# Kernel optimization log

Hardware: AMD Instinct MI355X
Metric: run time of the kernel (lower is better)

The kernel has to match this reference:

```python
import jax, jax.numpy as jnp
import numpy as np

EMBED_DIM = 2048
N_HEADS = 16
D_HEAD = EMBED_DIM // N_HEADS


def setup_inputs() -> dict:
    key = jax.random.key(0)
    kx, kq, kk, kv = jax.random.split(key, 4)
    B, N, D = 4, 2048, EMBED_DIM
    x = jax.random.normal(kx, (B, N, D), dtype=jnp.float32)
    Wq = jax.random.normal(kq, (D, D), dtype=jnp.float32) * 0.02
    Wk = jax.random.normal(kk, (D, D), dtype=jnp.float32) * 0.02
    Wv = jax.random.normal(kv, (D, D), dtype=jnp.float32) * 0.02
    return {"x": x, "Wq": Wq, "Wk": Wk, "Wv": Wv}


def reference(x, Wq, Wk, Wv):
    # x: [B, N, D]; weights applied as x @ W (matching torch.matmul in source)
    B, N, D = x.shape
    H, d = N_HEADS, D_HEAD
    # [B, N, D] -> [B, H, N, d]
    Q = (x @ Wq).reshape(B, N, H, d).transpose(0, 2, 1, 3)
    K = (x @ Wk).reshape(B, N, H, d).transpose(0, 2, 1, 3)
    V = (x @ Wv).reshape(B, N, H, d).transpose(0, 2, 1, 3)
    scale = 1.0 / jnp.sqrt(jnp.asarray(d, dtype=x.dtype))
    # non-causal SDPA (torch default: no mask, scale = 1/sqrt(d_head))
    scores = jnp.einsum('bhqd,bhkd->bhqk', Q, K) * scale  # [B,H,N,N]
    attn = jax.nn.softmax(scores, axis=-1)
    out = jnp.einsum('bhqk,bhkd->bhqd', attn, V)  # [B,H,N,d]
    return out
```

## Files before the change

### kernel.cpp

```cpp
#include <hip/hip_runtime.h>
#include <hip/hip_bf16.h>

#define B 4
#define N 2048
#define D 2048
#define H 16
#define DH 128
#define NT 32

typedef unsigned short u16;
typedef __attribute__((ext_vector_type(8))) short short8;
typedef __attribute__((ext_vector_type(4))) float floatx4;

__device__ __forceinline__ u16 f2b(float f) {
    union { __hip_bfloat16 h; u16 u; } cv;
    cv.h = __float2bfloat16(f);
    return cv.u;
}

__device__ __forceinline__ floatx4 mfma16(short8 a, short8 b, floatx4 c) {
    return __builtin_amdgcn_mfma_f32_16x16x32_bf16(a, b, c, 0, 0, 0);
}

#if __has_builtin(__builtin_amdgcn_exp2f)
#define EXP2(x) __builtin_amdgcn_exp2f(x)
#else
#define EXP2(x) exp2f(x)
#endif

__device__ __forceinline__ void async16(const void* g, void* l) {
    __builtin_amdgcn_global_load_lds(
        (const __attribute__((address_space(1))) unsigned int*)g,
        (__attribute__((address_space(3))) unsigned int*)l, 16, 0, 0);
}

__global__ __launch_bounds__(256) void cvt_x(const float* __restrict__ x,
                                             u16* __restrict__ xb) {
    size_t i = ((size_t)blockIdx.x * 256 + threadIdx.x) * 8;
    float4 v0 = *(const float4*)&x[i];
    float4 v1 = *(const float4*)&x[i + 4];
    union { u16 u[8]; uint4 s; } pk;
    pk.u[0] = f2b(v0.x); pk.u[1] = f2b(v0.y); pk.u[2] = f2b(v0.z); pk.u[3] = f2b(v0.w);
    pk.u[4] = f2b(v1.x); pk.u[5] = f2b(v1.y); pk.u[6] = f2b(v1.z); pk.u[7] = f2b(v1.w);
    *(uint4*)&xb[i] = pk.s;
}

__global__ __launch_bounds__(256) void cvt_w_t(const float* __restrict__ Wq,
                                               const float* __restrict__ Wk,
                                               const float* __restrict__ Wv,
                                               u16* __restrict__ wt) {
    __shared__ float tile[64][65];
    const int z = blockIdx.z;
    const float* W = (z == 0) ? Wq : (z == 1) ? Wk : Wv;
    const float scl = (z == 0) ? 0.12751743342f : 1.0f;
    const int k0 = blockIdx.x * 64, n0 = blockIdx.y * 64;
    const int tr = threadIdx.x >> 4, tc = threadIdx.x & 15;
#pragma unroll
    for (int i = 0; i < 4; i++) {
        int kk = tr + 16 * i;
        float4 vv = *(const float4*)&W[(size_t)(k0 + kk) * D + n0 + tc * 4];
        tile[kk][tc * 4 + 0] = vv.x; tile[kk][tc * 4 + 1] = vv.y;
        tile[kk][tc * 4 + 2] = vv.z; tile[kk][tc * 4 + 3] = vv.w;
    }
    __syncthreads();
#pragma unroll
    for (int i = 0; i < 4; i++) {
        int nn = tr + 16 * i;
        union { u16 u[4]; ushort4 s; } pk;
#pragma unroll
        for (int j = 0; j < 4; j++) pk.u[j] = f2b(tile[tc * 4 + j][nn] * scl);
        *(ushort4*)&wt[(size_t)z * D * D + (size_t)(n0 + nn) * D + k0 + tc * 4] = pk.s;
    }
}

#define KT 32
#define SGB __builtin_amdgcn_sched_group_barrier
__global__ __launch_bounds__(512, 2) void qkv_gemm(const u16* __restrict__ xb,
                                                   const u16* __restrict__ wt,
                                                   u16* __restrict__ qo,
                                                   u16* __restrict__ ko,
                                                   u16* __restrict__ vo) {
    __shared__ u16 lds[81920];

    const int bid = blockIdx.x;
    const int c = bid & 7, i = bid >> 3;
    const int i6 = (i * 43) >> 8;
    const int tm = ((c >> 2) << 4) + i6;
    const int tn = (c & 3) * 6 + (i - 6 * i6);

    const int t = threadIdx.x, lane = t & 63, w = t >> 6;
    const int wr = w >> 2, wc = w & 3;
    const int q4 = lane >> 4, lr = lane & 15;

    const int m0 = tm * 256;
    const int n0 = tn * 256;

    unsigned aoff[2][2], boff[2][2];
#pragma unroll
    for (int ii = 0; ii < 2; ii++) {
        const int off = ii * 8192 + w * 1024 + lane * 16;
        const int row = off >> 7;
        const int s = (off >> 4) & 7;
        const int col = ((s ^ (row & 7))) * 8;
#pragma unroll
        for (int h = 0; h < 2; h++) {
            aoff[h][ii] = (unsigned)((m0 + h * 128 + row) * D + col);
            boff[h][ii] = (unsigned)((n0 + h * 128 + row) * D + col);
        }
    }

    const unsigned cb0 = (unsigned)(((0 * 4 + q4) ^ (lr & 7)) * 16);
    const unsigned cb1 = (unsigned)(((1 * 4 + q4) ^ (lr & 7)) * 16);
    const unsigned aC0 = (unsigned)(wr * 16384 + lr * 128) + cb0;
    const unsigned aC1 = (unsigned)(wr * 16384 + lr * 128) + cb1;
    const unsigned bC0 = (unsigned)((wc >> 1) * 16384 + (wc & 1) * 8192 + lr * 128) + cb0;
    const unsigned bC1 = (unsigned)((wc >> 1) * 16384 + (wc & 1) * 8192 + lr * 128) + cb1;

#define STAGE_A(bufoff, h, j) {                                                           \
    async16(xb + aoff[h][0] + (unsigned)(j) * 64,                                         \
            (char*)lds + (bufoff) + (h) * 16384 + w * 1024);                              \
    async16(xb + aoff[h][1] + (unsigned)(j) * 64,                                         \
            (char*)lds + (bufoff) + (h) * 16384 + 8192 + w * 1024); }
#define STAGE_B(bufoff, h, j) {                                                           \
    async16(wt + boff[h][0] + (unsigned)(j) * 64,                                         \
            (char*)lds + (bufoff) + (h) * 16384 + w * 1024);                              \
    async16(wt + boff[h][1] + (unsigned)(j) * 64,                                         \
            (char*)lds + (bufoff) + (h) * 16384 + 8192 + w * 1024); }
#define BAR() __builtin_amdgcn_s_barrier()
#define DSR(off) (*(const short8*)((const char*)lds + (off)))

    floatx4 acc[8][4];
#pragma unroll
    for (int x = 0; x < 8; x++)
#pragma unroll
        for (int j = 0; j < 4; j++) acc[x][j] = (floatx4){0.f, 0.f, 0.f, 0.f};

    STAGE_A(0u, 0, 0); STAGE_A(0u, 1, 0);
    STAGE_B(98304u, 0, 0); STAGE_B(98304u, 1, 0);
    STAGE_A(32768u, 0, 1); STAGE_A(32768u, 1, 1);
    asm volatile("s_waitcnt vmcnt(4)" ::: "memory");
    BAR();

    unsigned aOffR = 0u;
    unsigned aOffW = 65536u;

    for (int g = 0; g < KT; g++) {
        const unsigned bR = 98304u + (unsigned)((g & 1) << 15);
        const unsigned bW = 98304u + (unsigned)(((g + 1) & 1) << 15);

        if (g + 1 < KT) { STAGE_B(bW, 0, g + 1); STAGE_B(bW, 1, g + 1); }
        if (g + 2 < KT) { STAGE_A(aOffW, 0, g + 2); STAGE_A(aOffW, 1, g + 2); }
        __builtin_amdgcn_sched_barrier(0);

        const unsigned aB0 = aOffR + aC0, aB1 = aOffR + aC1;
        const unsigned bB0 = bR + bC0, bB1 = bR + bC1;

        short8 a0k0[4], a0k1[4], a1k0[4], a1k1[4];
        short8 b0k0[2], b0k1[2], b1k0[2], b1k1[2];

        b0k0[0] = DSR(bB0);        b0k0[1] = DSR(bB0 + 2048);
#pragma unroll
        for (int mf = 0; mf < 4; mf++) a0k0[mf] = DSR(aB0 + mf * 2048);
#pragma unroll
        for (int mf = 0; mf < 4; mf++) a1k0[mf] = DSR(aB0 + 8192 + mf * 2048);
#pragma unroll
        for (int nf = 0; nf < 2; nf++)
#pragma unroll
            for (int mf = 0; mf < 4; mf++)
                acc[mf][nf] = mfma16(a0k0[mf], b0k0[nf], acc[mf][nf]);
        b1k0[0] = DSR(bB0 + 4096); b1k0[1] = DSR(bB0 + 6144);
#pragma unroll
        for (int nf = 0; nf < 2; nf++)
#pragma unroll
            for (int mf = 0; mf < 4; mf++)
                acc[4 + mf][nf] = mfma16(a1k0[mf], b0k0[nf], acc[4 + mf][nf]);
        b0k1[0] = DSR(bB1);        b0k1[1] = DSR(bB1 + 2048);
#pragma unroll
        for (int mf = 0; mf < 4; mf++) a0k1[mf] = DSR(aB1 + mf * 2048);
#pragma unroll
        for (int nf = 0; nf < 2; nf++)
#pragma unroll
            for (int mf = 0; mf < 4; mf++)
                acc[4 + mf][2 + nf] = mfma16(a1k0[mf], b1k0[nf], acc[4 + mf][2 + nf]);
#pragma unroll
        for (int mf = 0; mf < 4; mf++) a1k1[mf] = DSR(aB1 + 8192 + mf * 2048);
#pragma unroll
        for (int nf = 0; nf < 2; nf++)
#pragma unroll
            for (int mf = 0; mf < 4; mf++)
                acc[mf][2 + nf] = mfma16(a0k0[mf], b1k0[nf], acc[mf][2 + nf]);
        b1k1[0] = DSR(bB1 + 4096); b1k1[1] = DSR(bB1 + 6144);
#pragma unroll
        for (int nf = 0; nf < 2; nf++)
#pragma unroll
            for (int mf = 0; mf < 4; mf++)
                acc[mf][nf] = mfma16(a0k1[mf], b0k1[nf], acc[mf][nf]);
#pragma unroll
        for (int nf = 0; nf < 2; nf++)
#pragma unroll
            for (int mf = 0; mf < 4; mf++)
                acc[4 + mf][nf] = mfma16(a1k1[mf], b0k1[nf], acc[4 + mf][nf]);
#pragma unroll
        for (int nf = 0; nf < 2; nf++)
#pragma unroll
            for (int mf = 0; mf < 4; mf++)
                acc[4 + mf][2 + nf] = mfma16(a1k1[mf], b1k1[nf], acc[4 + mf][2 + nf]);
#pragma unroll
        for (int nf = 0; nf < 2; nf++)
#pragma unroll
            for (int mf = 0; mf < 4; mf++)
                acc[mf][2 + nf] = mfma16(a0k1[mf], b1k1[nf], acc[mf][2 + nf]);

        SGB(0x100, 10, 0);
        SGB(0x008,  8, 0);
        SGB(0x100,  2, 0);
        SGB(0x008,  8, 0);
        SGB(0x100,  6, 0);
        SGB(0x008,  8, 0);
        SGB(0x100,  4, 0);
        SGB(0x008,  8, 0);
        SGB(0x100,  2, 0);
        SGB(0x008,  8, 0);
        SGB(0x008,  8, 0);
        SGB(0x008,  8, 0);
        SGB(0x008,  8, 0);

        if (g == KT - 2) { asm volatile("s_waitcnt vmcnt(0)" ::: "memory"); }
        else if (g < KT - 2) { asm volatile("s_waitcnt vmcnt(4)" ::: "memory"); }
        if (g + 1 < KT) BAR();

        aOffR = (aOffR == 65536u) ? 0u : aOffR + 32768u;
        aOffW = (aOffW == 65536u) ? 0u : aOffW + 32768u;
    }

    const int z = tn >> 3;
    u16* dst = (z == 0) ? qo : (z == 1) ? ko : vo;
    const int c2b = (tn & 7) * 256 + wc * 64;
    const int grb = tm * 256 + wr * 128;
#pragma unroll
    for (int mf = 0; mf < 8; mf++)
#pragma unroll
        for (int nf = 0; nf < 4; nf++)
#pragma unroll
            for (int r = 0; r < 4; r++) {
                int gr = grb + mf * 16 + q4 * 4 + r;
                int c2 = c2b + nf * 16 + lr;
                int b_ = gr >> 11, n_ = gr & (N - 1);
                int head = c2 >> 7, dcol = c2 & 127;
                dst[((size_t)(b_ * H + head) * N + n_) * DH + dcol] = f2b(acc[mf][nf][r]);
            }
#undef STAGE_A
#undef STAGE_B
#undef BAR
#undef DSR
}

__global__ __launch_bounds__(256) void transpose_v(const u16* __restrict__ v,
                                                   u16* __restrict__ vt) {
    __shared__ u16 tile[64][72];
    const int bh = blockIdx.z;
    const int n0 = blockIdx.x * 64, d0 = blockIdx.y * 64;
    const int t = threadIdx.x;
#pragma unroll
    for (int i = 0; i < 2; i++) {
        int gid = t + 256 * i;
        int nl = gid >> 3, g = gid & 7;
        *(uint4*)&tile[nl][g * 8] =
            *(const uint4*)&v[((size_t)bh * N + n0 + nl) * DH + d0 + g * 8];
    }
    __syncthreads();
#pragma unroll
    for (int i = 0; i < 2; i++) {
        int gid = t + 256 * i;
        int dl = gid >> 3, gn = gid & 7;
        union { u16 u[8]; uint4 s; } pk;
#pragma unroll
        for (int j = 0; j < 8; j++) {
            int kp = gn * 8 + j;
            int src = 32 * (kp >> 5) + 16 * (kp & 1) + ((kp >> 1) & 15);
            pk.u[j] = tile[src][dl];
        }
        *(uint4*)&vt[((size_t)bh * DH + d0 + dl) * N + n0 + gn * 8] = pk.s;
    }
}

#define FMAX2 17.312340491f
__global__ __launch_bounds__(256, 2) void attn_kernel(const u16* __restrict__ q,
                                                      const u16* __restrict__ k,
                                                      const u16* __restrict__ vt,
                                                      float* __restrict__ out) {
    __shared__ u16 Ks[2][64][128];
    __shared__ u16 Vts[2][128][64];
    __shared__ u16 Ps[128][64];

    const int beta = blockIdx.x;
    const int bh = (beta & 7) + 8 * (beta >> 7);
    const int qt = (beta >> 3) & 15;
    const int t = threadIdx.x;
    const int w = t >> 6, lane = t & 63;
    const int half = lane >> 4, lr = lane & 15;
    const int a = w & 1, b = w >> 1;

    const size_t qbase = ((size_t)bh * N + (size_t)qt * 128) * DH;
    short8 af[4][4];
#pragma unroll
    for (int rt = 0; rt < 4; rt++)
#pragma unroll
        for (int ks = 0; ks < 4; ks++)
            af[rt][ks] = *(const short8*)&q[qbase + (size_t)(64 * b + 16 * rt + lr) * DH
                                            + ks * 32 + half * 8];

    float lrow[4][4];
    floatx4 o[4][4];
#pragma unroll
    for (int rt = 0; rt < 4; rt++)
#pragma unroll
        for (int r = 0; r < 4; r++) lrow[rt][r] = 0.f;
#pragma unroll
    for (int rt = 0; rt < 4; rt++)
#pragma unroll
        for (int ct = 0; ct < 4; ct++) o[rt][ct] = (floatx4){0.f, 0.f, 0.f, 0.f};

    const size_t kbase = (size_t)bh * N * DH;
    const size_t vtbase = (size_t)bh * DH * N;
    const u16* kp[4];
    const u16* vp[4];
#pragma unroll
    for (int c = 0; c < 4; c++) {
        int grp = 4 * w + c;
        int krow = 4 * grp + (lane >> 4);
        int kg = (lane & 15) ^ (krow & 15);
        kp[c] = &k[kbase + (size_t)krow * DH + kg * 8];
        int vrow = 8 * grp + (lane >> 3);
        int vg = (lane & 7) ^ (vrow & 7);
        vp[c] = &vt[vtbase + (size_t)vrow * N + vg * 8];
    }

#pragma unroll
    for (int c = 0; c < 4; c++) {
        async16(kp[c], (char*)&Ks[0][0][0] + (4 * w + c) * 1024);
        async16(vp[c], (char*)&Vts[0][0][0] + (4 * w + c) * 1024);
    }

    for (int kt = 0; kt < NT; kt++) {
        const int cur = kt & 1;
        __syncthreads();

        floatx4 sf[4][2];
#pragma unroll
        for (int ct = 0; ct < 2; ct++) {
            short8 bf[4];
#pragma unroll
            for (int ks = 0; ks < 4; ks++) {
                int gs = (4 * ks + half) ^ lr;
                bf[ks] = *(const short8*)&Ks[cur][32 * a + 16 * ct + lr][gs * 8];
            }
#pragma unroll
            for (int rt = 0; rt < 4; rt++) {
                floatx4 s = (floatx4){0.f, 0.f, 0.f, 0.f};
#pragma unroll
                for (int ks = 0; ks < 4; ks++) s = mfma16(af[rt][ks], bf[ks], s);
                sf[rt][ct] = s;
            }
        }

#pragma unroll
        for (int rt = 0; rt < 4; rt++)
#pragma unroll
            for (int r = 0; r < 4; r++) {
                int row = 64 * b + 16 * rt + 4 * half + r;
                float p0 = EXP2(sf[rt][0][r] - FMAX2);
                float p1 = EXP2(sf[rt][1][r] - FMAX2);
                lrow[rt][r] += p0 + p1;
                unsigned int pw = (unsigned int)f2b(p0) | ((unsigned int)f2b(p1) << 16);
                int u = (16 * a + lr) ^ ((row & 7) << 2);
                *(unsigned int*)&Ps[row][u * 2] = pw;
            }

        __syncthreads();

        if (kt + 1 < NT) {
            const int nb = cur ^ 1;
#pragma unroll
            for (int c = 0; c < 4; c++) {
                async16(kp[c] + (size_t)(kt + 1) * 64 * DH,
                        (char*)&Ks[nb][0][0] + (4 * w + c) * 1024);
                async16(vp[c] + (size_t)(kt + 1) * 64,
                        (char*)&Vts[nb][0][0] + (4 * w + c) * 1024);
            }
        }

#pragma unroll
        for (int ks = 0; ks < 2; ks++) {
            short8 a2[4];
#pragma unroll
            for (int rt = 0; rt < 4; rt++) {
                int g = (4 * ks + half) ^ (lr & 7);
                a2[rt] = *(const short8*)&Ps[64 * b + 16 * rt + lr][g * 8];
            }
#pragma unroll
            for (int ct = 0; ct < 4; ct++) {
                int dd = 64 * a + 16 * ct + lr;
                int gv = (4 * ks + half) ^ (lr & 7);
                short8 bv = *(const short8*)&Vts[cur][dd][gv * 8];
#pragma unroll
                for (int rt = 0; rt < 4; rt++)
                    o[rt][ct] = mfma16(a2[rt], bv, o[rt][ct]);
            }
        }
    }

    __syncthreads();
    float* Ls = (float*)&Ps[0][0];
#pragma unroll
    for (int rt = 0; rt < 4; rt++)
#pragma unroll
        for (int r = 0; r < 4; r++) {
            float s = lrow[rt][r];
            s += __shfl_xor(s, 1);
            s += __shfl_xor(s, 2);
            s += __shfl_xor(s, 4);
            s += __shfl_xor(s, 8);
            if (lr == 0) Ls[a * 128 + (64 * b + 16 * rt + 4 * half + r)] = s;
        }
    __syncthreads();
    const size_t obase = ((size_t)bh * N + (size_t)qt * 128) * DH;
#pragma unroll
    for (int rt = 0; rt < 4; rt++)
#pragma unroll
        for (int r = 0; r < 4; r++) {
            int row = 64 * b + 16 * rt + 4 * half + r;
            float inv = 1.f / (Ls[row] + Ls[128 + row]);
#pragma unroll
            for (int ct = 0; ct < 4; ct++)
                out[obase + (size_t)row * DH + 64 * a + 16 * ct + lr] = o[rt][ct][r] * inv;
        }
}

extern "C" void kernel_launch(void* const* d_in, const int* in_sizes, int n_in,
                              void* d_out, int out_size, void* d_ws, size_t ws_size,
                              hipStream_t stream) {
    const float* x  = (const float*)d_in[0];
    const float* Wq = (const float*)d_in[1];
    const float* Wk = (const float*)d_in[2];
    const float* Wv = (const float*)d_in[3];
    float* out = (float*)d_out;
    char* ws = (char*)d_ws;

    u16* xb = (u16*)(ws);
    u16* wt = (u16*)(ws + 33554432);
    u16* qb = (u16*)(ws + 58720256);
    u16* kb = (u16*)(ws + 92274688);
    u16* vb = (u16*)(ws + 125829120);
    u16* vtb = (u16*)(ws);

    cvt_x<<<dim3(8192), dim3(256), 0, stream>>>(x, xb);
    cvt_w_t<<<dim3(32, 32, 3), dim3(256), 0, stream>>>(Wq, Wk, Wv, wt);
    qkv_gemm<<<dim3(768), dim3(512), 0, stream>>>(xb, wt, qb, kb, vb);
    transpose_v<<<dim3(32, 2, 64), dim3(256), 0, stream>>>(vb, vtb);
    attn_kernel<<<dim3(1024), dim3(256), 0, stream>>>(qb, kb, vtb, out);
}
```

Measured before the change: 463.4 us.

## Keep P in registers via transposed QK MFMA and split-K PV reduction

The QK^T MFMA now runs with swapped operands, so each lane's score outputs already form the A-operand layout the PV MFMA needs. The P tile therefore stays in registers instead of going through a shared-memory round trip, and one barrier per iteration is dropped. To match this, the V-transpose permutation is changed, warps split the key dimension and each accumulates all 128 output columns, and a final shared-memory reduction combines the two halves. The cost is a doubled output accumulator (more registers, which may hurt occupancy at launch bounds of 2) plus an extra epilogue reduction. The next-tile prefetch is also issued earlier in each iteration.

```diff
diff --git a/kernel.cpp b/kernel.cpp
--- a/kernel.cpp
+++ b/kernel.cpp
@@ -277,7 +277,7 @@
 #pragma unroll
         for (int j = 0; j < 8; j++) {
             int kp = gn * 8 + j;
-            int src = 32 * (kp >> 5) + 16 * (kp & 1) + ((kp >> 1) & 15);
+            int src = 32 * (kp >> 5) + 16 * ((kp >> 2) & 1) + 4 * ((kp >> 3) & 3) + (kp & 3);
             pk.u[j] = tile[src][dl];
         }
         *(uint4*)&vt[((size_t)bh * DH + d0 + dl) * N + n0 + gn * 8] = pk.s;
@@ -289,16 +289,14 @@
                                                       const u16* __restrict__ k,
                                                       const u16* __restrict__ vt,
                                                       float* __restrict__ out) {
-    __shared__ u16 Ks[2][64][128];
-    __shared__ u16 Vts[2][128][64];
-    __shared__ u16 Ps[128][64];
+    __shared__ __align__(16) char smem[66560];
 
     const int beta = blockIdx.x;
     const int bh = (beta & 7) + 8 * (beta >> 7);
     const int qt = (beta >> 3) & 15;
     const int t = threadIdx.x;
     const int w = t >> 6, lane = t & 63;
-    const int half = lane >> 4, lr = lane & 15;
+    const int q4 = lane >> 4, lr = lane & 15;
     const int a = w & 1, b = w >> 1;
 
     const size_t qbase = ((size_t)bh * N + (size_t)qt * 128) * DH;
@@ -308,133 +306,161 @@
 #pragma unroll
         for (int ks = 0; ks < 4; ks++)
             af[rt][ks] = *(const short8*)&q[qbase + (size_t)(64 * b + 16 * rt + lr) * DH
-                                            + ks * 32 + half * 8];
-
-    float lrow[4][4];
-    floatx4 o[4][4];
+                                            + ks * 32 + q4 * 8];
+
+    float lrow[4] = {0.f, 0.f, 0.f, 0.f};
+    floatx4 o[4][8];
 #pragma unroll
     for (int rt = 0; rt < 4; rt++)
 #pragma unroll
-        for (int r = 0; r < 4; r++) lrow[rt][r] = 0.f;
-#pragma unroll
-    for (int rt = 0; rt < 4; rt++)
-#pragma unroll
-        for (int ct = 0; ct < 4; ct++) o[rt][ct] = (floatx4){0.f, 0.f, 0.f, 0.f};
-
-    const size_t kbase = (size_t)bh * N * DH;
-    const size_t vtbase = (size_t)bh * DH * N;
-    const u16* kp[4];
-    const u16* vp[4];
+        for (int cv = 0; cv < 8; cv++) o[rt][cv] = (floatx4){0.f, 0.f, 0.f, 0.f};
+
+    const u16* kpB = k + (size_t)bh * N * DH;
+    const u16* vpB = vt + (size_t)bh * DH * N;
+    unsigned koff[4], voff[4];
 #pragma unroll
     for (int c = 0; c < 4; c++) {
         int grp = 4 * w + c;
         int krow = 4 * grp + (lane >> 4);
         int kg = (lane & 15) ^ (krow & 15);
-        kp[c] = &k[kbase + (size_t)krow * DH + kg * 8];
+        koff[c] = (unsigned)(krow * DH + kg * 8);
         int vrow = 8 * grp + (lane >> 3);
         int vg = (lane & 7) ^ (vrow & 7);
-        vp[c] = &vt[vtbase + (size_t)vrow * N + vg * 8];
-    }
+        voff[c] = (unsigned)(vrow * N + vg * 8);
+    }
+
+    unsigned kaddr[4];
+#pragma unroll
+    for (int ks = 0; ks < 4; ks++)
+        kaddr[ks] = (unsigned)((32 * a + lr) * 256 + (((4 * ks + q4) ^ lr) * 16));
+    unsigned vaddr = (unsigned)(32768 + lr * 128 + (((4 * a + q4) ^ (lr & 7)) * 16));
 
 #pragma unroll
     for (int c = 0; c < 4; c++) {
-        async16(kp[c], (char*)&Ks[0][0][0] + (4 * w + c) * 1024);
-        async16(vp[c], (char*)&Vts[0][0][0] + (4 * w + c) * 1024);
+        async16(kpB + koff[c], smem + (4 * w + c) * 1024);
+        async16(vpB + voff[c], smem + 32768 + (4 * w + c) * 1024);
     }
 
     for (int kt = 0; kt < NT; kt++) {
-        const int cur = kt & 1;
         __syncthreads();
 
-        floatx4 sf[4][2];
-#pragma unroll
-        for (int ct = 0; ct < 2; ct++) {
+        if (kt + 1 < NT) {
+            const int nb = (kt + 1) & 1;
+#pragma unroll
+            for (int c = 0; c < 4; c++) {
+                async16(kpB + koff[c] + (unsigned)(kt + 1) * 64 * DH,
+                        smem + nb * 16384 + (4 * w + c) * 1024);
+                async16(vpB + voff[c] + (unsigned)(kt + 1) * 64,
+                        smem + 32768 + nb * 16384 + (4 * w + c) * 1024);
+            }
+        }
+
+        unsigned paw[4][4];
+        {
             short8 bf[4];
 #pragma unroll
-            for (int ks = 0; ks < 4; ks++) {
-                int gs = (4 * ks + half) ^ lr;
-                bf[ks] = *(const short8*)&Ks[cur][32 * a + 16 * ct + lr][gs * 8];
-            }
+            for (int ks = 0; ks < 4; ks++)
+                bf[ks] = *(const short8*)(smem + kaddr[ks]);
 #pragma unroll
             for (int rt = 0; rt < 4; rt++) {
                 floatx4 s = (floatx4){0.f, 0.f, 0.f, 0.f};
 #pragma unroll
-                for (int ks = 0; ks < 4; ks++) s = mfma16(af[rt][ks], bf[ks], s);
-                sf[rt][ct] = s;
-            }
-        }
-
+                for (int ks = 0; ks < 4; ks++) s = mfma16(bf[ks], af[rt][ks], s);
+                float p0 = EXP2(s[0] - FMAX2), p1 = EXP2(s[1] - FMAX2);
+                float p2 = EXP2(s[2] - FMAX2), p3 = EXP2(s[3] - FMAX2);
+                lrow[rt] += (p0 + p1) + (p2 + p3);
+                paw[rt][0] = (unsigned)f2b(p0) | ((unsigned)f2b(p1) << 16);
+                paw[rt][1] = (unsigned)f2b(p2) | ((unsigned)f2b(p3) << 16);
+            }
+#pragma unroll
+            for (int ks = 0; ks < 4; ks++)
+                bf[ks] = *(const short8*)(smem + kaddr[ks] + 4096);
+#pragma unroll
+            for (int rt = 0; rt < 4; rt++) {
+                floatx4 s = (floatx4){0.f, 0.f, 0.f, 0.f};
+#pragma unroll
+                for (int ks = 0; ks < 4; ks++) s = mfma16(bf[ks], af[rt][ks], s);
+                float p0 = EXP2(s[0] - FMAX2), p1 = EXP2(s[1] - FMAX2);
+                float p2 = EXP2(s[2] - FMAX2), p3 = EXP2(s[3] - FMAX2);
+                lrow[rt] += (p0 + p1) + (p2 + p3);
+                paw[rt][2] = (unsigned)f2b(p0) | ((unsigned)f2b(p1) << 16);
+                paw[rt][3] = (unsigned)f2b(p2) | ((unsigned)f2b(p3) << 16);
+            }
+        }
+        short8 PA[4];
+#pragma unroll
+        for (int rt = 0; rt < 4; rt++) {
+            union { unsigned uu[4]; short8 s8; } cv_;
+            cv_.uu[0] = paw[rt][0]; cv_.uu[1] = paw[rt][1];
+            cv_.uu[2] = paw[rt][2]; cv_.uu[3] = paw[rt][3];
+            PA[rt] = cv_.s8;
+        }
+
+#pragma unroll
+        for (int ctv = 0; ctv < 8; ctv++) {
+            short8 bv = *(const short8*)(smem + vaddr + ctv * 2048);
+#pragma unroll
+            for (int rt = 0; rt < 4; rt++)
+                o[rt][ctv] = mfma16(PA[rt], bv, o[rt][ctv]);
+        }
+
+#pragma unroll
+        for (int ks = 0; ks < 4; ks++) kaddr[ks] ^= 16384u;
+        vaddr ^= 16384u;
+    }
+
+    __syncthreads();
+    float* Ls = (float*)smem;
+#pragma unroll
+    for (int rt = 0; rt < 4; rt++) {
+        float s = lrow[rt];
+        s += __shfl_xor(s, 16);
+        s += __shfl_xor(s, 32);
+        if (q4 == 0) Ls[a * 128 + 64 * b + 16 * rt + lr] = s;
+    }
+    __syncthreads();
+
+    floatx4 inv4[4];
+#pragma unroll
+    for (int rt = 0; rt < 4; rt++)
+#pragma unroll
+        for (int r = 0; r < 4; r++) {
+            int row = 64 * b + 16 * rt + 4 * q4 + r;
+            inv4[rt][r] = 1.f / (Ls[row] + Ls[128 + row]);
+        }
+
+    char* Ox = smem + 1024;
+    if (a == 1) {
 #pragma unroll
         for (int rt = 0; rt < 4; rt++)
 #pragma unroll
-            for (int r = 0; r < 4; r++) {
-                int row = 64 * b + 16 * rt + 4 * half + r;
-                float p0 = EXP2(sf[rt][0][r] - FMAX2);
-                float p1 = EXP2(sf[rt][1][r] - FMAX2);
-                lrow[rt][r] += p0 + p1;
-                unsigned int pw = (unsigned int)f2b(p0) | ((unsigned int)f2b(p1) << 16);
-                int u = (16 * a + lr) ^ ((row & 7) << 2);
-                *(unsigned int*)&Ps[row][u * 2] = pw;
-            }
-
-        __syncthreads();
-
-        if (kt + 1 < NT) {
-            const int nb = cur ^ 1;
-#pragma unroll
-            for (int c = 0; c < 4; c++) {
-                async16(kp[c] + (size_t)(kt + 1) * 64 * DH,
-                        (char*)&Ks[nb][0][0] + (4 * w + c) * 1024);
-                async16(vp[c] + (size_t)(kt + 1) * 64,
-                        (char*)&Vts[nb][0][0] + (4 * w + c) * 1024);
-            }
-        }
-
-#pragma unroll
-        for (int ks = 0; ks < 2; ks++) {
-            short8 a2[4];
-#pragma unroll
-            for (int rt = 0; rt < 4; rt++) {
-                int g = (4 * ks + half) ^ (lr & 7);
-                a2[rt] = *(const short8*)&Ps[64 * b + 16 * rt + lr][g * 8];
-            }
-#pragma unroll
-            for (int ct = 0; ct < 4; ct++) {
-                int dd = 64 * a + 16 * ct + lr;
-                int gv = (4 * ks + half) ^ (lr & 7);
-                short8 bv = *(const short8*)&Vts[cur][dd][gv * 8];
-#pragma unroll
-                for (int rt = 0; rt < 4; rt++)
-                    o[rt][ct] = mfma16(a2[rt], bv, o[rt][ct]);
-            }
-        }
-    }
-
+            for (int ctv = 0; ctv < 8; ctv++) {
+                int dd = 16 * ctv + lr;
+                int slot = (16 * b + 4 * rt + q4) ^ (dd & 31);
+                floatx4 v = o[rt][ctv];
+                v[0] *= inv4[rt][0]; v[1] *= inv4[rt][1];
+                v[2] *= inv4[rt][2]; v[3] *= inv4[rt][3];
+                *(floatx4*)(Ox + dd * 512 + slot * 16) = v;
+            }
+    }
     __syncthreads();
-    float* Ls = (float*)&Ps[0][0];
-#pragma unroll
-    for (int rt = 0; rt < 4; rt++)
-#pragma unroll
-        for (int r = 0; r < 4; r++) {
-            float s = lrow[rt][r];
-            s += __shfl_xor(s, 1);
-            s += __shfl_xor(s, 2);
-            s += __shfl_xor(s, 4);
-            s += __shfl_xor(s, 8);
-            if (lr == 0) Ls[a * 128 + (64 * b + 16 * rt + 4 * half + r)] = s;
-        }
-    __syncthreads();
-    const size_t obase = ((size_t)bh * N + (size_t)qt * 128) * DH;
-#pragma unroll
-    for (int rt = 0; rt < 4; rt++)
-#pragma unroll
-        for (int r = 0; r < 4; r++) {
-            int row = 64 * b + 16 * rt + 4 * half + r;
-            float inv = 1.f / (Ls[row] + Ls[128 + row]);
-#pragma unroll
-            for (int ct = 0; ct < 4; ct++)
-                out[obase + (size_t)row * DH + 64 * a + 16 * ct + lr] = o[rt][ct][r] * inv;
-        }
+    if (a == 0) {
+        const size_t obase = ((size_t)bh * N + (size_t)qt * 128) * DH;
+#pragma unroll
+        for (int rt = 0; rt < 4; rt++)
+#pragma unroll
+            for (int ctv = 0; ctv < 8; ctv++) {
+                int dd = 16 * ctv + lr;
+                int slot = (16 * b + 4 * rt + q4) ^ (dd & 31);
+                floatx4 vx = *(const floatx4*)(Ox + dd * 512 + slot * 16);
+#pragma unroll
+                for (int r = 0; r < 4; r++) {
+                    int row = 64 * b + 16 * rt + 4 * q4 + r;
+                    out[obase + (size_t)row * DH + dd] =
+                        o[rt][ctv][r] * inv4[rt][r] + vx[r];
+                }
+            }
+    }
 }
 
 extern "C" void kernel_launch(void* const* d_in, const int* in_sizes, int n_in,
```

New measurement: 543.6 us. 1.17x slower.
